# Kernel tuning notes

Hardware: AMD Instinct MI355X
Metric: run time of the kernel (lower is better)

The kernel has to match this reference:

```python
import jax, jax.numpy as jnp
import numpy as np
from jax import lax

D_MODEL, D_INNER, D_STATE, D_CONV, DT_RANK = 128, 256, 16, 4, 8
BATCH, SEQ = 8, 4096


def setup_inputs() -> dict:
    key = jax.random.key(0)
    ks = jax.random.split(key, 13)
    g = lambda k, shape, fan: (jax.random.normal(k, shape, jnp.float32) / np.sqrt(fan)).astype(jnp.float32)
    inp = {
        "s": jax.random.normal(ks[0], (BATCH, SEQ, D_MODEL), jnp.float32),
        "in_proj_w": g(ks[1], (2 * D_INNER, D_MODEL), D_MODEL),
        "conv_w": g(ks[2], (D_INNER, 1, D_CONV), D_CONV),
        "conv_b": jnp.zeros((D_INNER,), jnp.float32),
        "x_proj_w": g(ks[3], (DT_RANK + 2 * D_STATE, D_INNER), D_INNER),
        "dt_proj_w": g(ks[4], (D_INNER, DT_RANK), DT_RANK),
        "dt_proj_b": jax.random.uniform(ks[5], (D_INNER,), jnp.float32, -4.0, -2.0),  # softplus(b) small, like mamba dt init
        "A_log": jnp.log(jnp.broadcast_to(jnp.arange(1, D_STATE + 1, dtype=jnp.float32), (D_INNER, D_STATE))),
        "D_skip": jnp.ones((D_INNER,), jnp.float32),
        "out_proj_w": g(ks[6], (D_MODEL, D_INNER), D_INNER),
        "ln_gamma": jnp.ones((D_MODEL,), jnp.float32),
        "ln_beta": jnp.zeros((D_MODEL,), jnp.float32),
        "fc_w": g(ks[7], (D_MODEL, D_MODEL), D_MODEL),
    }
    return inp


def _mamba(s, in_proj_w, conv_w, conv_b, x_proj_w, dt_proj_w, dt_proj_b, A_log, D_skip, out_proj_w):
    B, L, _ = s.shape
    xz = jnp.einsum("bld,ed->ble", s, in_proj_w)           # [B,L,2*D_INNER]
    x, z = jnp.split(xz, 2, axis=-1)                        # each [B,L,D_INNER]
    # causal depthwise conv1d
    xc = jnp.transpose(x, (0, 2, 1))                        # [B,D_INNER,L]
    xc = jnp.pad(xc, ((0, 0), (0, 0), (D_CONV - 1, 0)))
    xc = lax.conv_general_dilated(xc, conv_w, (1,), "VALID",
                                  dimension_numbers=("NCH", "OIH", "NCH"),
                                  feature_group_count=D_INNER)
    x = jax.nn.silu(jnp.transpose(xc + conv_b[None, :, None], (0, 2, 1)))  # [B,L,D_INNER]
    # input-dependent dt, B, C
    x_dbl = jnp.einsum("bld,ed->ble", x, x_proj_w)
    dt = x_dbl[..., :DT_RANK]
    Bc = x_dbl[..., DT_RANK:DT_RANK + D_STATE]              # [B,L,D_STATE]
    Cc = x_dbl[..., DT_RANK + D_STATE:]                     # [B,L,D_STATE]
    dt = jax.nn.softplus(jnp.einsum("blr,dr->bld", dt, dt_proj_w) + dt_proj_b)  # [B,L,D_INNER]
    A = -jnp.exp(A_log)                                     # [D_INNER,D_STATE]

    def step(h, inp):
        dt_t, b_t, c_t, u_t = inp                           # [B,Di],[B,Ds],[B,Ds],[B,Di]
        dA = jnp.exp(dt_t[:, :, None] * A)                  # [B,Di,Ds]
        dBu = (dt_t * u_t)[:, :, None] * b_t[:, None, :]
        h = dA * h + dBu
        y = jnp.einsum("bds,bs->bd", h, c_t)
        return h, y

    h0 = jnp.zeros((B, D_INNER, D_STATE), x.dtype)
    xs = (jnp.swapaxes(dt, 0, 1), jnp.swapaxes(Bc, 0, 1), jnp.swapaxes(Cc, 0, 1), jnp.swapaxes(x, 0, 1))
    _, ys = lax.scan(step, h0, xs)                          # ys: [L,B,D_INNER]
    y = jnp.swapaxes(ys, 0, 1) + x * D_skip
    y = y * jax.nn.silu(z)
    return jnp.einsum("bld,od->blo", y, out_proj_w)         # [B,L,D_MODEL]


def reference(s, in_proj_w, conv_w, conv_b, x_proj_w, dt_proj_w, dt_proj_b, A_log, D_skip, out_proj_w, ln_gamma, ln_beta, fc_w):
    h = _mamba(s, in_proj_w, conv_w, conv_b, x_proj_w, dt_proj_w, dt_proj_b, A_log, D_skip, out_proj_w)
    mu = jnp.mean(h, axis=-1, keepdims=True)
    var = jnp.mean(jnp.square(h - mu), axis=-1, keepdims=True)
    hn = (h - mu) * lax.rsqrt(var + 1e-5) * ln_gamma + ln_beta
    return jax.nn.relu(jnp.einsum("bld,od->blo", hn, fc_w))
```

## Files before the change

### kernel.cpp

```cpp
#include <hip/hip_runtime.h>
#include <math.h>

#define B_ 8
#define L_ 4096
#define DM 128
#define DI 256
#define DSN 16
#define RK 8
#define M_ (B_*L_)
#define NC 128
#define CH 32
#define CH2 64

typedef __attribute__((ext_vector_type(8))) short bfrag;
typedef __attribute__((ext_vector_type(4))) float ffrag;
typedef __attribute__((ext_vector_type(2))) float f32x2;

__device__ __forceinline__ float silu_f(float x) {
  return x * __builtin_amdgcn_rcpf(1.f + __expf(-x));
}
__device__ __forceinline__ float softplus_f(float x) {
  return (x > 20.f) ? x : __logf(1.f + __expf(x));
}

__device__ __forceinline__ unsigned short f2bf(float f) {
  unsigned int u = __builtin_bit_cast(unsigned int, f);
  unsigned int r = (u + 0x7FFFu + ((u >> 16) & 1u)) >> 16;
  return (unsigned short)r;
}
__device__ __forceinline__ unsigned int f2bf2(float lo, float hi) {
  return (unsigned int)f2bf(lo) | ((unsigned int)f2bf(hi) << 16);
}
__device__ __forceinline__ float bf2f(unsigned int us) {
  return __builtin_bit_cast(float, us << 16);
}

__global__ __launch_bounds__(256)
void gemm_bf16_in(const float* __restrict__ A, const float* __restrict__ W,
                  unsigned short* __restrict__ xb, unsigned short* __restrict__ zsb) {
  __shared__ unsigned short As[64 * 136];
  __shared__ unsigned short Ws[64 * 136];
  __shared__ unsigned short Os[64 * 72];
  const int t = threadIdx.x;
  const int m0 = blockIdx.y << 6;
  const int half = blockIdx.x;
  unsigned short* __restrict__ outp = half ? zsb : xb;
  const float* __restrict__ Wbase = W + (half << 8) * 128;
  for (int i = t; i < 64 * 32; i += 256) {
    int row = i >> 5, c4 = i & 31;
    float4 av = *(const float4*)&A[(m0 + row) * 128 + (c4 << 2)];
    uint2 ap = {f2bf2(av.x, av.y), f2bf2(av.z, av.w)};
    *(uint2*)&As[row * 136 + (c4 << 2)] = ap;
  }
  float4 wr[8];
#pragma unroll
  for (int k = 0; k < 8; ++k) {
    int i = t + (k << 8);
    int row = i >> 5, c4 = i & 31;
    wr[k] = *(const float4*)&Wbase[row * 128 + (c4 << 2)];
  }
#pragma unroll
  for (int k = 0; k < 8; ++k) {
    int i = t + (k << 8);
    int row = i >> 5, c4 = i & 31;
    uint2 wp = {f2bf2(wr[k].x, wr[k].y), f2bf2(wr[k].z, wr[k].w)};
    *(uint2*)&Ws[row * 136 + (c4 << 2)] = wp;
  }
  __syncthreads();
  const int w = t >> 6, l = t & 63, q = l >> 4, col = l & 15;
  for (int jt = 0; jt < 4; ++jt) {
    if (jt < 3) {
#pragma unroll
      for (int k = 0; k < 8; ++k) {
        int i = t + (k << 8);
        int row = i >> 5, c4 = i & 31;
        wr[k] = *(const float4*)&Wbase[(((jt + 1) << 6) + row) * 128 + (c4 << 2)];
      }
    }
    ffrag acc[4] = {{0.f,0.f,0.f,0.f},{0.f,0.f,0.f,0.f},{0.f,0.f,0.f,0.f},{0.f,0.f,0.f,0.f}};
#pragma unroll
    for (int s = 0; s < 4; ++s) {
      int k0 = s * 32 + q * 8;
      bfrag af = *(const bfrag*)&As[((w << 4) + col) * 136 + k0];
#pragma unroll
      for (int nt = 0; nt < 4; ++nt) {
        bfrag bf_ = *(const bfrag*)&Ws[((nt << 4) + col) * 136 + k0];
        acc[nt] = __builtin_amdgcn_mfma_f32_16x16x32_bf16(af, bf_, acc[nt], 0, 0, 0);
      }
    }
    __syncthreads();
#pragma unroll
    for (int nt = 0; nt < 4; ++nt)
#pragma unroll
      for (int i = 0; i < 4; ++i) {
        int ml = (w << 4) + (q << 2) + i;
        float v = acc[nt][i];
        if (half) v = silu_f(v);
        Os[ml * 72 + (nt << 4) + col] = f2bf(v);
      }
    if (jt < 3) {
#pragma unroll
      for (int k = 0; k < 8; ++k) {
        int i = t + (k << 8);
        int row = i >> 5, c4 = i & 31;
        uint2 wp = {f2bf2(wr[k].x, wr[k].y), f2bf2(wr[k].z, wr[k].w)};
        *(uint2*)&Ws[row * 136 + (c4 << 2)] = wp;
      }
    }
    __syncthreads();
    {
      int r = t >> 2, c8 = (t & 3) << 3;
      int m = m0 + r;
      *(uint4*)&outp[m * 256 + (jt << 6) + c8]      = *(const uint4*)&Os[r * 72 + c8];
      *(uint4*)&outp[m * 256 + (jt << 6) + 32 + c8] = *(const uint4*)&Os[r * 72 + 32 + c8];
    }
  }
}

__global__ __launch_bounds__(512)
void xproj_dtproj(const unsigned short* __restrict__ xb, const float* __restrict__ xw,
                  const float* __restrict__ dtw, const float* __restrict__ dtpb,
                  const float* __restrict__ cw, const float* __restrict__ cb,
                  float* __restrict__ Bb, float* __restrict__ Cb,
                  unsigned int* __restrict__ udt) {
  __shared__ unsigned short ua[64 * 264];
  __shared__ unsigned short wb[48 * 264];
  __shared__ float dtr_s[64 * 12];
  const int t = threadIdx.x;
  const int p0 = blockIdx.x << 6;
  {
    const int k = t & 255, half = t >> 8;
    const int pstart = half << 5;
    const int base = p0 + pstart;
    const int lb = base & (L_ - 1);
    const float w0 = cw[k*4], w1 = cw[k*4+1], w2 = cw[k*4+2], w3 = cw[k*4+3];
    const float bias = cb[k];
    float x0 = (lb >= 3) ? bf2f((unsigned int)xb[(base - 3) * 256 + k]) : 0.f;
    float x1 = (lb >= 2) ? bf2f((unsigned int)xb[(base - 2) * 256 + k]) : 0.f;
    float x2 = (lb >= 1) ? bf2f((unsigned int)xb[(base - 1) * 256 + k]) : 0.f;
#pragma unroll 8
    for (int it = 0; it < 32; ++it) {
      float x3 = bf2f((unsigned int)xb[(base + it) * 256 + k]);
      float u = silu_f(fmaf(w0, x0, fmaf(w1, x1, fmaf(w2, x2, fmaf(w3, x3, bias)))));
      ua[(pstart + it) * 264 + k] = f2bf(u);
      x0 = x1; x1 = x2; x2 = x3;
    }
  }
  for (int i = t; i < 40 * 256; i += 512) {
    int n = i >> 8, k = i & 255;
    wb[n * 264 + k] = f2bf(xw[i]);
  }
  for (int i = t; i < 8 * 264; i += 512) wb[40 * 264 + i] = 0;
  __syncthreads();
  const int w = t >> 6, l = t & 63, q = l >> 4, col = l & 15;
  for (int tile = w; tile < 12; tile += 8) {
    const int mt = tile & 3, nt = tile >> 2;
    ffrag acc = {0.f, 0.f, 0.f, 0.f};
#pragma unroll
    for (int s = 0; s < 8; ++s) {
      int k0 = s * 32 + q * 8;
      bfrag af = *(const bfrag*)&ua[((mt << 4) + col) * 264 + k0];
      bfrag bf_ = *(const bfrag*)&wb[((nt << 4) + col) * 264 + k0];
      acc = __builtin_amdgcn_mfma_f32_16x16x32_bf16(af, bf_, acc, 0, 0, 0);
    }
#pragma unroll
    for (int i = 0; i < 4; ++i) {
      int ml = (mt << 4) + (q << 2) + i;
      int m = p0 + ml;
      if (nt == 0) {
        if (col < 8) dtr_s[ml * 12 + col] = acc[i];
        else         Bb[m * 16 + (col - 8)] = acc[i];
      } else if (nt == 1) {
        if (col < 8) Bb[m * 16 + 8 + col] = acc[i];
        else         Cb[m * 16 + (col - 8)] = acc[i];
      } else {
        if (col < 8) Cb[m * 16 + 8 + col] = acc[i];
      }
    }
  }
  __syncthreads();
  {
    const int d = t & 255, half = t >> 8;
    const int pstart = half << 5;
    float w8[8];
    *(float4*)&w8[0] = *(const float4*)&dtw[d * 8];
    *(float4*)&w8[4] = *(const float4*)&dtw[d * 8 + 4];
    const float bias = dtpb[d];
#pragma unroll 4
    for (int pp = pstart; pp < pstart + 32; ++pp) {
      float r0[8];
      *(float4*)&r0[0] = *(const float4*)&dtr_s[pp * 12];
      *(float4*)&r0[4] = *(const float4*)&dtr_s[pp * 12 + 4];
      float a2 = bias;
#pragma unroll
      for (int r2 = 0; r2 < 8; ++r2) a2 = fmaf(r0[r2], w8[r2], a2);
      float sp = softplus_f(a2);
      udt[(p0 + pp) * 256 + d] =
          (unsigned int)ua[pp * 264 + d] | ((unsigned int)f2bf(sp) << 16);
    }
  }
}

__global__ __launch_bounds__(512, 4)
void scan_phase1(const unsigned int* __restrict__ udt,
                 const float* __restrict__ Bb, const float* __restrict__ alog,
                 unsigned short* __restrict__ cP, unsigned short* __restrict__ cHe) {
  __shared__ float Bs[CH * 16];
  const int bc = blockIdx.x;
  const int b = bc >> 7, c = bc & (NC - 1);
  const int t = threadIdx.x;
  const int l = t & 63, w = t >> 6;
  const int d = (w << 5) + (l & 31);
  const int sh = l >> 5;
  const int soff = sh << 3;
  const int base = b * L_ + c * CH;
  if (t < CH * 4) ((float4*)Bs)[t] = *(const float4*)&Bb[base * 16 + (t << 2)];
  float a[8];
  bool okl = true;
#pragma unroll
  for (int j = 0; j < 8; ++j) {
    a[j] = -__expf(alog[d * 16 + soff + j]);
    float tgt = (float)(soff + j + 1);
    okl = okl && (fabsf(a[j] + tgt) <= 1e-3f * tgt);
  }
  const bool fast = (bool)__all((int)okl);
  f32x2 h2[4] = {{0.f,0.f},{0.f,0.f},{0.f,0.f},{0.f,0.f}};
  float sdt = 0.f;
  unsigned int wv0 = udt[base * 256 + d];
  unsigned int wv1 = udt[(base + 1) * 256 + d];
  __syncthreads();
#pragma unroll 4
  for (int ll = 0; ll < CH; ++ll) {
    const int m2 = base + ((ll + 2 < CH) ? ll + 2 : CH - 1);
    unsigned int wv2 = udt[m2 * 256 + d];
    float4 b0 = *(const float4*)&Bs[ll * 16 + soff];
    float4 b1 = *(const float4*)&Bs[ll * 16 + soff + 4];
    float uv  = bf2f(wv0 & 0xFFFFu);
    float dtv = bf2f(wv0 >> 16);
    f32x2 B2[4] = {{b0.x,b0.y},{b0.z,b0.w},{b1.x,b1.y},{b1.z,b1.w}};
    float du = dtv * uv;
    sdt += dtv;
    if (fast) {
      float e1 = __expf(-dtv);
      float e2 = e1 * e1, e4 = e2 * e2, e8 = e4 * e4;
      float st = sh ? e8 * e1 : e1;
      f32x2 dA = {st, st * e1};
      f32x2 e22 = {e2, e2};
      f32x2 du2 = {du, du};
#pragma unroll
      for (int j = 0; j < 4; ++j) {
        h2[j] = dA * h2[j] + du2 * B2[j];
        dA = dA * e22;
      }
    } else {
#pragma unroll
      for (int j = 0; j < 8; ++j) {
        float dA = __expf(dtv * a[j]);
        h2[j >> 1][j & 1] = fmaf(dA, h2[j >> 1][j & 1], du * B2[j >> 1][j & 1]);
      }
    }
    wv0 = wv1; wv1 = wv2;
  }
#pragma unroll
  for (int j = 0; j < 8; ++j) {
    int o = (bc * 16 + soff + j) * 256 + d;
    cP[o]  = f2bf(__expf(a[j] * sdt));
    cHe[o] = f2bf(h2[j >> 1][j & 1]);
  }
}

__global__ __launch_bounds__(512)
void scan_combine(unsigned short* __restrict__ cP, const unsigned short* __restrict__ cHe) {
  __shared__ float segP[64 * 9], segH[64 * 9], segS[64 * 9];
  const int t = threadIdx.x;
  const int sdl = t & 63, seg = t >> 6;
  const int blk = blockIdx.x;
  const int b = blk >> 6, grp = blk & 63;
  const int sd = (grp << 6) + sdl;
  const int base = b * NC * 4096 + sd;
  float Pacc = 1.f, Hacc = 0.f;
#pragma unroll
  for (int i = 0; i < 16; ++i) {
    int idx = base + (seg * 16 + i) * 4096;
    float p = bf2f((unsigned int)cP[idx]);
    float he = bf2f((unsigned int)cHe[idx]);
    Hacc = fmaf(p, Hacc, he);
    Pacc *= p;
  }
  segP[sdl * 9 + seg] = Pacc;
  segH[sdl * 9 + seg] = Hacc;
  __syncthreads();
  if (t < 64) {
    float hs = 0.f;
#pragma unroll
    for (int s2 = 0; s2 < 8; ++s2) {
      segS[t * 9 + s2] = hs;
      hs = fmaf(segP[t * 9 + s2], hs, segH[t * 9 + s2]);
    }
  }
  __syncthreads();
  float hs = segS[sdl * 9 + seg];
#pragma unroll
  for (int i = 0; i < 16; ++i) {
    int idx = base + (seg * 16 + i) * 4096;
    float p = bf2f((unsigned int)cP[idx]);
    float he = bf2f((unsigned int)cHe[idx]);
    cP[idx] = f2bf(hs);
    hs = fmaf(p, hs, he);
  }
}

__global__ __launch_bounds__(512, 4)
void scan3_out_ln_fc(const unsigned int* __restrict__ udt,
                     const float* __restrict__ Bb, const float* __restrict__ Cb,
                     const float* __restrict__ alog, const unsigned short* __restrict__ hst,
                     const float* __restrict__ dsk,
                     const unsigned short* __restrict__ zsb,
                     const float* __restrict__ W,
                     const float* __restrict__ gamma, const float* __restrict__ beta,
                     const float* __restrict__ fcw, float* __restrict__ out) {
  __shared__ float Bs[CH2 * 16];
  __shared__ float Cs[CH2 * 16];
  __shared__ unsigned short smA[64 * 264];
  __shared__ unsigned short smB[128 * 136];
  const int bc = blockIdx.x;
  const int b = bc >> 6, cc = bc & 63;
  const int t = threadIdx.x;
  const int l = t & 63, w = t >> 6;
  const int d = (w << 5) + (l & 31);
  const int sh = l >> 5;
  const int soff = sh << 3;
  const int base = b * L_ + (cc << 1) * CH;
  const int hc = b * NC + (cc << 1);
  if (t < CH2 * 4)           ((float4*)Bs)[t]            = *(const float4*)&Bb[base * 16 + (t << 2)];
  else if (t < CH2 * 8)      ((float4*)Cs)[t - CH2 * 4]  = *(const float4*)&Cb[base * 16 + ((t - CH2 * 4) << 2)];
  float a[8];
  bool okl = true;
#pragma unroll
  for (int j = 0; j < 8; ++j) {
    a[j] = -__expf(alog[d * 16 + soff + j]);
    float tgt = (float)(soff + j + 1);
    okl = okl && (fabsf(a[j] + tgt) <= 1e-3f * tgt);
  }
  const bool fast = (bool)__all((int)okl);
  const float dskv = dsk[d];
  f32x2 h2[4];
#pragma unroll
  for (int j = 0; j < 8; ++j)
    h2[j >> 1][j & 1] = bf2f((unsigned int)hst[(hc * 16 + soff + j) * 256 + d]);
  unsigned int wv0 = udt[base * 256 + d];
  unsigned int wv1 = udt[(base + 1) * 256 + d];
  unsigned short zv0 = zsb[base * 256 + d];
  unsigned short zv1 = zsb[(base + 1) * 256 + d];
  __syncthreads();
#pragma unroll 4
  for (int ll = 0; ll < CH2; ++ll) {
    const int m2 = base + ((ll + 2 < CH2) ? ll + 2 : CH2 - 1);
    unsigned int wv2 = udt[m2 * 256 + d];
    unsigned short zv2 = zsb[m2 * 256 + d];
    float4 b0 = *(const float4*)&Bs[ll * 16 + soff];
    float4 b1 = *(const float4*)&Bs[ll * 16 + soff + 4];
    float4 c0 = *(const float4*)&Cs[ll * 16 + soff];
    float4 c1 = *(const float4*)&Cs[ll * 16 + soff + 4];
    float uv  = bf2f(wv0 & 0xFFFFu);
    float dtv = bf2f(wv0 >> 16);
    f32x2 B2[4] = {{b0.x,b0.y},{b0.z,b0.w},{b1.x,b1.y},{b1.z,b1.w}};
    f32x2 C2[4] = {{c0.x,c0.y},{c0.z,c0.w},{c1.x,c1.y},{c1.z,c1.w}};
    float du = dtv * uv;
    f32x2 y2 = {0.f, 0.f};
    if (fast) {
      float e1 = __expf(-dtv);
      float e2 = e1 * e1, e4 = e2 * e2, e8 = e4 * e4;
      float st = sh ? e8 * e1 : e1;
      f32x2 dA = {st, st * e1};
      f32x2 e22 = {e2, e2};
      f32x2 du2 = {du, du};
#pragma unroll
      for (int j = 0; j < 4; ++j) {
        h2[j] = dA * h2[j] + du2 * B2[j];
        y2 = y2 + h2[j] * C2[j];
        dA = dA * e22;
      }
    } else {
#pragma unroll
      for (int j = 0; j < 8; ++j) {
        float dA = __expf(dtv * a[j]);
        float hh = fmaf(dA, h2[j >> 1][j & 1], du * B2[j >> 1][j & 1]);
        h2[j >> 1][j & 1] = hh;
        y2[j & 1] = fmaf(hh, C2[j >> 1][j & 1], y2[j & 1]);
      }
    }
    float y = y2.x + y2.y;
    y += __shfl_xor(y, 32);
    if (sh == 0) {
      float zs = bf2f((unsigned int)zv0);
      smA[ll * 264 + d] = f2bf(fmaf(uv, dskv, y) * zs);
    }
    wv0 = wv1; wv1 = wv2; zv0 = zv1; zv1 = zv2;
  }
  const int q = l >> 4, col = l & 15;
  ffrag acc[2][4];
  for (int nt2 = 0; nt2 < 2; ++nt2) {
    __syncthreads();
    for (int i = t; i < 64 * 64; i += 512) {
      int row = i >> 6, c4 = i & 63;
      float4 wv = *(const float4*)&W[((nt2 << 6) + row) * 256 + (c4 << 2)];
      uint2 wp = {f2bf2(wv.x, wv.y), f2bf2(wv.z, wv.w)};
      *(uint2*)&smB[row * 264 + (c4 << 2)] = wp;
    }
    __syncthreads();
    if (t < 256) {
#pragma unroll
      for (int nt = 0; nt < 4; ++nt) acc[nt2][nt] = (ffrag){0.f, 0.f, 0.f, 0.f};
#pragma unroll
      for (int s = 0; s < 8; ++s) {
        int k0 = s * 32 + q * 8;
        bfrag af = *(const bfrag*)&smA[((w << 4) + col) * 264 + k0];
#pragma unroll
        for (int nt = 0; nt < 4; ++nt) {
          bfrag bf_ = *(const bfrag*)&smB[((nt << 4) + col) * 264 + k0];
          acc[nt2][nt] = __builtin_amdgcn_mfma_f32_16x16x32_bf16(af, bf_, acc[nt2][nt], 0, 0, 0);
        }
      }
    }
  }
  float mu[4], rs[4];
  if (t < 256) {
#pragma unroll
    for (int i = 0; i < 4; ++i) {
      float s1 = 0.f, s2 = 0.f;
#pragma unroll
      for (int nt2 = 0; nt2 < 2; ++nt2)
#pragma unroll
        for (int nt = 0; nt < 4; ++nt) {
          float v = acc[nt2][nt][i];
          s1 += v; s2 = fmaf(v, v, s2);
        }
      s1 += __shfl_xor(s1, 1); s2 += __shfl_xor(s2, 1);
      s1 += __shfl_xor(s1, 2); s2 += __shfl_xor(s2, 2);
      s1 += __shfl_xor(s1, 4); s2 += __shfl_xor(s2, 4);
      s1 += __shfl_xor(s1, 8); s2 += __shfl_xor(s2, 8);
      mu[i] = s1 * (1.f / DM);
      float var = s2 * (1.f / DM) - mu[i] * mu[i];
      rs[i] = rsqrtf(var + 1e-5f);
    }
  }
  __syncthreads();
  if (t < 256) {
#pragma unroll
    for (int nt2 = 0; nt2 < 2; ++nt2)
#pragma unroll
      for (int nt = 0; nt < 4; ++nt) {
        int n = (nt2 << 6) + (nt << 4) + col;
        float g = gamma[n], be = beta[n];
#pragma unroll
        for (int i = 0; i < 4; ++i) {
          int r = (w << 4) + (q << 2) + i;
          smA[r * 136 + n] = f2bf(fmaf((acc[nt2][nt][i] - mu[i]) * rs[i], g, be));
        }
      }
  }
  for (int i = t; i < 128 * 32; i += 512) {
    int row = i >> 5, c4 = i & 31;
    float4 wv = *(const float4*)&fcw[row * 128 + (c4 << 2)];
    uint2 wp = {f2bf2(wv.x, wv.y), f2bf2(wv.z, wv.w)};
    *(uint2*)&smB[row * 136 + (c4 << 2)] = wp;
  }
  __syncthreads();
  if (t < 256) {
    ffrag a2[8] = {{0.f,0.f,0.f,0.f},{0.f,0.f,0.f,0.f},{0.f,0.f,0.f,0.f},{0.f,0.f,0.f,0.f},
                   {0.f,0.f,0.f,0.f},{0.f,0.f,0.f,0.f},{0.f,0.f,0.f,0.f},{0.f,0.f,0.f,0.f}};
#pragma unroll
    for (int s = 0; s < 4; ++s) {
      int k0 = s * 32 + q * 8;
      bfrag af = *(const bfrag*)&smA[((w << 4) + col) * 136 + k0];
#pragma unroll
      for (int nt = 0; nt < 8; ++nt) {
        bfrag bf_ = *(const bfrag*)&smB[((nt << 4) + col) * 136 + k0];
        a2[nt] = __builtin_amdgcn_mfma_f32_16x16x32_bf16(af, bf_, a2[nt], 0, 0, 0);
      }
    }
#pragma unroll
    for (int nt = 0; nt < 8; ++nt)
#pragma unroll
      for (int i = 0; i < 4; ++i) {
        int ml = (w << 4) + (q << 2) + i;
        out[(base + ml) * 128 + (nt << 4) + col] = fmaxf(a2[nt][i], 0.f);
      }
  }
}

extern "C" void kernel_launch(void* const* d_in, const int* in_sizes, int n_in,
                              void* d_out, int out_size, void* d_ws, size_t ws_size,
                              hipStream_t stream) {
  (void)in_sizes; (void)n_in; (void)out_size; (void)ws_size;
  const float* s    = (const float*)d_in[0];
  const float* w_in = (const float*)d_in[1];
  const float* cw   = (const float*)d_in[2];
  const float* cb   = (const float*)d_in[3];
  const float* xw   = (const float*)d_in[4];
  const float* dtw  = (const float*)d_in[5];
  const float* dtpb = (const float*)d_in[6];
  const float* alog = (const float*)d_in[7];
  const float* dsk  = (const float*)d_in[8];
  const float* ow   = (const float*)d_in[9];
  const float* gam  = (const float*)d_in[10];
  const float* bet  = (const float*)d_in[11];
  const float* fcw  = (const float*)d_in[12];
  float* out = (float*)d_out;
  float* ws  = (float*)d_ws;

  unsigned short* xb   = (unsigned short*)ws;
  unsigned short* zsb  = (unsigned short*)(ws + 4194304);
  unsigned int*   udt  = (unsigned int*)(ws + 8388608);
  float*          Bb   = ws + 16777216;
  float*          Cb   = ws + 17301504;
  unsigned short* cP   = (unsigned short*)(ws + 17825792);
  unsigned short* cHe  = (unsigned short*)(ws + 19922944);

  gemm_bf16_in<<<dim3(2, 512), 256, 0, stream>>>(s, w_in, xb, zsb);
  xproj_dtproj<<<512, 512, 0, stream>>>(xb, xw, dtw, dtpb, cw, cb, Bb, Cb, udt);
  scan_phase1<<<B_ * NC, 512, 0, stream>>>(udt, Bb, alog, cP, cHe);
  scan_combine<<<512, 512, 0, stream>>>(cP, cHe);
  scan3_out_ln_fc<<<B_ * NC / 2, 512, 0, stream>>>(udt, Bb, Cb, alog, cP, dsk, zsb,
                                                   ow, gam, bet, fcw, out);
}
```

Before: 186.0 us.

## Split scan3 across two chunks per block, one thread owning all 16 states

After: 178.5 us. -4.0%, faster.

```diff
diff --git a/kernel.cpp b/kernel.cpp
--- a/kernel.cpp
+++ b/kernel.cpp
@@ -201,7 +201,7 @@
   }
 }
 
-__global__ __launch_bounds__(512, 4)
+__global__ __launch_bounds__(512, 8)
 void scan_phase1(const unsigned int* __restrict__ udt,
                  const float* __restrict__ Bb, const float* __restrict__ alog,
                  unsigned short* __restrict__ cP, unsigned short* __restrict__ cHe) {
@@ -327,63 +327,72 @@
   const int b = bc >> 6, cc = bc & 63;
   const int t = threadIdx.x;
   const int l = t & 63, w = t >> 6;
-  const int d = (w << 5) + (l & 31);
-  const int sh = l >> 5;
-  const int soff = sh << 3;
+  const int chh = t >> 8;
+  const int d = t & 255;
   const int base = b * L_ + (cc << 1) * CH;
-  const int hc = b * NC + (cc << 1);
+  const int cbase = base + chh * CH;
+  const int hc = b * NC + (cc << 1) + chh;
   if (t < CH2 * 4)           ((float4*)Bs)[t]            = *(const float4*)&Bb[base * 16 + (t << 2)];
   else if (t < CH2 * 8)      ((float4*)Cs)[t - CH2 * 4]  = *(const float4*)&Cb[base * 16 + ((t - CH2 * 4) << 2)];
-  float a[8];
+  float a[16];
   bool okl = true;
 #pragma unroll
-  for (int j = 0; j < 8; ++j) {
-    a[j] = -__expf(alog[d * 16 + soff + j]);
-    float tgt = (float)(soff + j + 1);
+  for (int j = 0; j < 16; ++j) {
+    a[j] = -__expf(alog[d * 16 + j]);
+    float tgt = (float)(j + 1);
     okl = okl && (fabsf(a[j] + tgt) <= 1e-3f * tgt);
   }
   const bool fast = (bool)__all((int)okl);
   const float dskv = dsk[d];
-  f32x2 h2[4];
-#pragma unroll
-  for (int j = 0; j < 8; ++j)
-    h2[j >> 1][j & 1] = bf2f((unsigned int)hst[(hc * 16 + soff + j) * 256 + d]);
-  unsigned int wv0 = udt[base * 256 + d];
-  unsigned int wv1 = udt[(base + 1) * 256 + d];
-  unsigned short zv0 = zsb[base * 256 + d];
-  unsigned short zv1 = zsb[(base + 1) * 256 + d];
-  __syncthreads();
-#pragma unroll 4
-  for (int ll = 0; ll < CH2; ++ll) {
-    const int m2 = base + ((ll + 2 < CH2) ? ll + 2 : CH2 - 1);
-    unsigned int wv2 = udt[m2 * 256 + d];
-    unsigned short zv2 = zsb[m2 * 256 + d];
-    float4 b0 = *(const float4*)&Bs[ll * 16 + soff];
-    float4 b1 = *(const float4*)&Bs[ll * 16 + soff + 4];
-    float4 c0 = *(const float4*)&Cs[ll * 16 + soff];
-    float4 c1 = *(const float4*)&Cs[ll * 16 + soff + 4];
+  f32x2 h2[8];
+#pragma unroll
+  for (int jj = 0; jj < 8; ++jj) {
+    h2[jj][0] = bf2f((unsigned int)hst[(hc * 16 + (jj << 1)) * 256 + d]);
+    h2[jj][1] = bf2f((unsigned int)hst[(hc * 16 + (jj << 1) + 1) * 256 + d]);
+  }
+  unsigned int wv0 = udt[cbase * 256 + d];
+  unsigned int wv1 = udt[(cbase + 1) * 256 + d];
+  unsigned short zv0 = zsb[cbase * 256 + d];
+  unsigned short zv1 = zsb[(cbase + 1) * 256 + d];
+  __syncthreads();
+#pragma unroll 2
+  for (int ll = 0; ll < CH; ++ll) {
+    const int l2 = (ll + 2 < CH) ? ll + 2 : CH - 1;
+    unsigned int wv2 = udt[(cbase + l2) * 256 + d];
+    unsigned short zv2 = zsb[(cbase + l2) * 256 + d];
+    const float* brow = &Bs[(chh * CH + ll) * 16];
+    const float* crow = &Cs[(chh * CH + ll) * 16];
+    float4 b0 = *(const float4*)&brow[0];
+    float4 b1 = *(const float4*)&brow[4];
+    float4 b2 = *(const float4*)&brow[8];
+    float4 b3 = *(const float4*)&brow[12];
+    float4 c0 = *(const float4*)&crow[0];
+    float4 c1 = *(const float4*)&crow[4];
+    float4 c2 = *(const float4*)&crow[8];
+    float4 c3 = *(const float4*)&crow[12];
     float uv  = bf2f(wv0 & 0xFFFFu);
     float dtv = bf2f(wv0 >> 16);
-    f32x2 B2[4] = {{b0.x,b0.y},{b0.z,b0.w},{b1.x,b1.y},{b1.z,b1.w}};
-    f32x2 C2[4] = {{c0.x,c0.y},{c0.z,c0.w},{c1.x,c1.y},{c1.z,c1.w}};
+    f32x2 B2[8] = {{b0.x,b0.y},{b0.z,b0.w},{b1.x,b1.y},{b1.z,b1.w},
+                   {b2.x,b2.y},{b2.z,b2.w},{b3.x,b3.y},{b3.z,b3.w}};
+    f32x2 C2[8] = {{c0.x,c0.y},{c0.z,c0.w},{c1.x,c1.y},{c1.z,c1.w},
+                   {c2.x,c2.y},{c2.z,c2.w},{c3.x,c3.y},{c3.z,c3.w}};
     float du = dtv * uv;
+    f32x2 du2 = {du, du};
     f32x2 y2 = {0.f, 0.f};
     if (fast) {
       float e1 = __expf(-dtv);
-      float e2 = e1 * e1, e4 = e2 * e2, e8 = e4 * e4;
-      float st = sh ? e8 * e1 : e1;
-      f32x2 dA = {st, st * e1};
+      float e2 = e1 * e1;
+      f32x2 dA = {e1, e2};
       f32x2 e22 = {e2, e2};
-      f32x2 du2 = {du, du};
-#pragma unroll
-      for (int j = 0; j < 4; ++j) {
-        h2[j] = dA * h2[j] + du2 * B2[j];
-        y2 = y2 + h2[j] * C2[j];
+#pragma unroll
+      for (int jj = 0; jj < 8; ++jj) {
+        h2[jj] = dA * h2[jj] + du2 * B2[jj];
+        y2 = y2 + h2[jj] * C2[jj];
         dA = dA * e22;
       }
     } else {
 #pragma unroll
-      for (int j = 0; j < 8; ++j) {
+      for (int j = 0; j < 16; ++j) {
         float dA = __expf(dtv * a[j]);
         float hh = fmaf(dA, h2[j >> 1][j & 1], du * B2[j >> 1][j & 1]);
         h2[j >> 1][j & 1] = hh;
@@ -391,11 +400,8 @@
       }
     }
     float y = y2.x + y2.y;
-    y += __shfl_xor(y, 32);
-    if (sh == 0) {
-      float zs = bf2f((unsigned int)zv0);
-      smA[ll * 264 + d] = f2bf(fmaf(uv, dskv, y) * zs);
-    }
+    float zs = bf2f((unsigned int)zv0);
+    smA[(chh * CH + ll) * 264 + d] = f2bf(fmaf(uv, dskv, y) * zs);
     wv0 = wv1; wv1 = wv2; zv0 = zv1; zv1 = zv2;
   }
   const int q = l >> 4, col = l & 15;
```
